# Performance work log

Measured on AMD Instinct MI355X. Metric: run time of the kernel, lower is better.

The kernel has to match this reference:

```python
import jax, jax.numpy as jnp
import numpy as np

N_NODES = 100000
N_EDGES = 1600000
NUM_FEATURES = 512
HIDDEN = 128
NUM_CLASSES = 40


def setup_inputs() -> dict:
    key = jax.random.key(0)
    ks = jax.random.split(key, 6)
    x = jax.random.normal(ks[0], (N_NODES, NUM_FEATURES), dtype=jnp.float32)
    edge_index = jax.random.randint(ks[1], (2, N_EDGES), 0, N_NODES, dtype=jnp.int32)
    W1 = jax.random.normal(ks[2], (NUM_FEATURES, HIDDEN), dtype=jnp.float32) * 0.05
    b1 = jnp.zeros((HIDDEN,), dtype=jnp.float32)
    W2 = jax.random.normal(ks[3], (HIDDEN, NUM_CLASSES), dtype=jnp.float32) * 0.05
    b2 = jnp.zeros((NUM_CLASSES,), dtype=jnp.float32)
    return {"x": x, "edge_index": edge_index, "W1": W1, "b1": b1, "W2": W2, "b2": b2}


def _gcn_conv(x, W, b, src, dst, n):
    # PyG GCNConv: h = W x; out = D^{-1/2} (A + I) D^{-1/2} h + b
    h = x @ W                                            # [N, out]
    deg = jax.ops.segment_sum(jnp.ones(src.shape[0], h.dtype), dst,
                              num_segments=n) + 1.0      # +1 for self loop
    inv_sqrt = jax.lax.rsqrt(deg)                        # [N]
    coef = inv_sqrt[src] * inv_sqrt[dst]                 # [E]
    msgs = h[src] * coef[:, None]                        # [E, out] gather
    agg = jax.ops.segment_sum(msgs, dst, num_segments=n) # scatter-add
    agg = agg + h * (inv_sqrt * inv_sqrt)[:, None]       # self-loop term
    return agg + b


def reference(x, edge_index, W1, b1, W2, b2):
    src, dst = edge_index[0], edge_index[1]
    n = x.shape[0]
    h = jax.nn.relu(_gcn_conv(x, W1, b1, src, dst, n))
    # F.dropout(training=self.training): eval mode -> identity
    out = _gcn_conv(h, W2, b2, src, dst, n)
    return jax.nn.log_softmax(out, axis=1)
```

## Files before the change

### kernel.cpp

```cpp
#include <hip/hip_runtime.h>
#include <hip/hip_bf16.h>
#include <math.h>

#define N_NODES 100000
#define N_EDGES 1600000
#define F_IN 512
#define HID 128
#define NCLS 40
#define DEG_CAP 64
#define GM 128
#define NGB 782

typedef __attribute__((ext_vector_type(8))) short short8;
typedef __attribute__((ext_vector_type(4))) float floatx4;

__device__ __forceinline__ unsigned short f2bf(float x) {
    unsigned u = __builtin_bit_cast(unsigned, x);
    unsigned r = (u + 0x7FFFu + ((u >> 16) & 1u)) >> 16;
    return (unsigned short)r;
}
__device__ __forceinline__ float bflo(unsigned u) {
    return __builtin_bit_cast(float, u << 16);
}
__device__ __forceinline__ float bfhi(unsigned u) {
    return __builtin_bit_cast(float, u & 0xFFFF0000u);
}


__global__ __launch_bounds__(256) void k_prep(
    const float* __restrict__ W1, unsigned short* __restrict__ W1t,
    const float* __restrict__ W2, unsigned short* __restrict__ W2th,
    unsigned short* __restrict__ W2tl, int* __restrict__ cursor) {
    int b = blockIdx.x;
    if (b < 256) {
        int idx = b * 256 + threadIdx.x;
        int n = idx >> 9, k = idx & 511;
        W1t[idx] = f2bf(W1[k * HID + n]);
    } else if (b < 280) {
        int idx = (b - 256) * 256 + threadIdx.x;
        int n = idx >> 7, k = idx & 127;
        float v = (n < NCLS) ? W2[k * NCLS + n] : 0.f;
        unsigned short hi = f2bf(v);
        unsigned short lo = f2bf(v - bflo(hi));
        W2th[idx] = hi;
        W2tl[idx] = lo;
    } else {
        int i = (b - 280) * 256 + threadIdx.x;
        if (i < N_NODES) cursor[i] = 0;
    }
}


__global__ __launch_bounds__(256) void k_fused_g1f(
    const float* __restrict__ A,
    const unsigned short* __restrict__ Bt,
    unsigned short* __restrict__ C,
    int M,
    const int* __restrict__ src, const int* __restrict__ dst,
    int* __restrict__ cursor, int* __restrict__ csr)
{
    __shared__ unsigned short Asl[128 * 40];
    __shared__ unsigned short Bsl[128 * 40];

    if (blockIdx.x >= NGB) {
        int i = (blockIdx.x - NGB) * 256 + threadIdx.x;
        int d = dst[i];
        int pos = atomicAdd(&cursor[d], 1);
        if (pos < DEG_CAP) csr[((size_t)d << 6) + pos] = src[i];
        return;
    }

    const int tid  = threadIdx.x;
    const int wave = tid >> 6;
    const int lane = tid & 63;
    const int quad = lane >> 4;
    const int l15  = lane & 15;
    const int wm   = (wave >> 1) * 64;
    const int wn   = (wave & 1) * 64;
    const int block_m = blockIdx.x * GM;

    floatx4 acc[4][4];
    #pragma unroll
    for (int i = 0; i < 4; ++i)
        #pragma unroll
        for (int j = 0; j < 4; ++j) acc[i][j] = (floatx4){0.f, 0.f, 0.f, 0.f};

    for (int k0 = 0; k0 < F_IN; k0 += 32) {
        #pragma unroll
        for (int i = 0; i < 4; ++i) {
            int f  = tid + 256 * i;
            int r  = f >> 3;
            int kq = f & 7;
            int gr = block_m + r;
            gr = gr < M ? gr : M - 1;
            floatx4 v = *(const floatx4*)&A[(size_t)gr * F_IN + k0 + kq * 4];
            unsigned lo = (unsigned)f2bf(v.x) | ((unsigned)f2bf(v.y) << 16);
            unsigned hi = (unsigned)f2bf(v.z) | ((unsigned)f2bf(v.w) << 16);
            *(uint2*)&Asl[r * 40 + kq * 4] = make_uint2(lo, hi);
        }
        #pragma unroll
        for (int i = 0; i < 2; ++i) {
            int f  = tid + 256 * i;
            int r  = f >> 2;
            int kq = f & 3;
            int4 v = *(const int4*)&Bt[(size_t)r * F_IN + k0 + kq * 8];
            *(int4*)&Bsl[r * 40 + kq * 8] = v;
        }
        __syncthreads();

        short8 af[4], bfr[4];
        #pragma unroll
        for (int t = 0; t < 4; ++t)
            af[t] = *(const short8*)&Asl[(wm + t * 16 + l15) * 40 + quad * 8];
        #pragma unroll
        for (int t = 0; t < 4; ++t)
            bfr[t] = *(const short8*)&Bsl[(wn + t * 16 + l15) * 40 + quad * 8];

        #pragma unroll
        for (int tm = 0; tm < 4; ++tm)
            #pragma unroll
            for (int tn = 0; tn < 4; ++tn)
                acc[tm][tn] = __builtin_amdgcn_mfma_f32_16x16x32_bf16(
                    af[tm], bfr[tn], acc[tm][tn], 0, 0, 0);
        __syncthreads();
    }

    #pragma unroll
    for (int tm = 0; tm < 4; ++tm) {
        #pragma unroll
        for (int r = 0; r < 4; ++r) {
            int row = block_m + wm + tm * 16 + quad * 4 + r;
            if (row < M) {
                #pragma unroll
                for (int tn = 0; tn < 4; ++tn)
                    C[(size_t)row * HID + wn + tn * 16 + l15] =
                        f2bf(acc[tm][tn][r]);
            }
        }
    }
}

__global__ void k_inv(const int* __restrict__ deg, float* __restrict__ inv, int n) {
    int i = blockIdx.x * blockDim.x + threadIdx.x;
    if (i < n) inv[i] = rsqrtf((float)deg[i] + 1.0f);
}


__global__ __launch_bounds__(256) void k_gather1(
    const unsigned* __restrict__ h1s,
    const int* __restrict__ deg,
    const float* __restrict__ inv, const int* __restrict__ csr,
    const float* __restrict__ b1, float* __restrict__ hrelu)
{
    const int wave = threadIdx.x >> 6;
    const int lane = threadIdx.x & 63;
    const int node = blockIdx.x * 4 + wave;
    const int start = node << 6;
    const float invd = inv[node];
    int cnt = deg[node];
    cnt = cnt < DEG_CAP ? cnt : DEG_CAP;

    unsigned u = h1s[(size_t)node * 64 + lane];
    float acc0 = bflo(u) * invd, acc1 = bfhi(u) * invd;

    int t = 0;
    for (; t + 4 <= cnt; t += 4) {
        int s0 = csr[start + t + 0];
        int s1 = csr[start + t + 1];
        int s2 = csr[start + t + 2];
        int s3 = csr[start + t + 3];
        float w0 = inv[s0], w1 = inv[s1], w2 = inv[s2], w3 = inv[s3];
        unsigned u0 = h1s[(size_t)s0 * 64 + lane];
        unsigned u1 = h1s[(size_t)s1 * 64 + lane];
        unsigned u2 = h1s[(size_t)s2 * 64 + lane];
        unsigned u3 = h1s[(size_t)s3 * 64 + lane];
        acc0 += (bflo(u0) * w0 + bflo(u1) * w1) + (bflo(u2) * w2 + bflo(u3) * w3);
        acc1 += (bfhi(u0) * w0 + bfhi(u1) * w1) + (bfhi(u2) * w2 + bfhi(u3) * w3);
    }
    for (; t < cnt; ++t) {
        int s = csr[start + t];
        float w = inv[s];
        unsigned uu = h1s[(size_t)s * 64 + lane];
        acc0 += bflo(uu) * w;
        acc1 += bfhi(uu) * w;
    }

    float2 b = *(const float2*)&b1[lane * 2];
    float v0 = fmaxf(acc0 * invd + b.x, 0.f);
    float v1 = fmaxf(acc1 * invd + b.y, 0.f);
    *(float2*)&hrelu[(size_t)node * HID + lane * 2] = make_float2(v0, v1);
}


#define G2M 128

__global__ __launch_bounds__(256) void k_gemm2_mfma(
    const float* __restrict__ H,
    const unsigned short* __restrict__ Bh,
    const unsigned short* __restrict__ Bl,
    const float* __restrict__ inv,
    unsigned short* __restrict__ C,
    int M)
{
    __shared__ unsigned short Ahs[128 * 40];
    __shared__ unsigned short Als[128 * 40];
    __shared__ unsigned short Bhs[48 * 136];
    __shared__ unsigned short Bls[48 * 136];

    const int tid  = threadIdx.x;
    const int wave = tid >> 6;
    const int lane = tid & 63;
    const int quad = lane >> 4;
    const int l15  = lane & 15;
    const int wm   = wave * 32;
    const int block_m = blockIdx.x * G2M;

    for (int i = tid; i < 768; i += 256) {
        int n = i >> 4;
        int k = (i & 15) * 8;
        *(int4*)&Bhs[n * 136 + k] = *(const int4*)&Bh[n * 128 + k];
        *(int4*)&Bls[n * 136 + k] = *(const int4*)&Bl[n * 128 + k];
    }

    const int ra = tid >> 3, kqa = tid & 7;
    size_t aoff[4];
    #pragma unroll
    for (int i = 0; i < 4; ++i) {
        int gr = block_m + ra + 32 * i;
        gr = gr < M ? gr : M - 1;
        aoff[i] = (size_t)gr * HID + kqa * 4;
    }

    floatx4 hreg[4];
    #pragma unroll
    for (int i = 0; i < 4; ++i) hreg[i] = *(const floatx4*)&H[aoff[i]];

    floatx4 acc[2][3];
    #pragma unroll
    for (int i = 0; i < 2; ++i)
        #pragma unroll
        for (int j = 0; j < 3; ++j) acc[i][j] = (floatx4){0.f, 0.f, 0.f, 0.f};

    for (int step = 0; step < 4; ++step) {
        #pragma unroll
        for (int i = 0; i < 4; ++i) {
            floatx4 v = hreg[i];
            unsigned short hx = f2bf(v.x), hy = f2bf(v.y);
            unsigned short hz = f2bf(v.z), hw = f2bf(v.w);
            unsigned short lx = f2bf(v.x - bflo(hx));
            unsigned short ly = f2bf(v.y - bflo(hy));
            unsigned short lz = f2bf(v.z - bflo(hz));
            unsigned short lw = f2bf(v.w - bflo(hw));
            *(uint2*)&Ahs[(ra + 32 * i) * 40 + kqa * 4] =
                make_uint2((unsigned)hx | ((unsigned)hy << 16),
                           (unsigned)hz | ((unsigned)hw << 16));
            *(uint2*)&Als[(ra + 32 * i) * 40 + kqa * 4] =
                make_uint2((unsigned)lx | ((unsigned)ly << 16),
                           (unsigned)lz | ((unsigned)lw << 16));
        }
        __syncthreads();

        if (step < 3) {
            const int k1 = (step + 1) * 32;
            #pragma unroll
            for (int i = 0; i < 4; ++i) hreg[i] = *(const floatx4*)&H[aoff[i] + k1];
        }

        const int k0 = step * 32;
        short8 ah[2], al[2], bh[3], bl[3];
        #pragma unroll
        for (int t = 0; t < 2; ++t) {
            ah[t] = *(const short8*)&Ahs[(wm + t * 16 + l15) * 40 + quad * 8];
            al[t] = *(const short8*)&Als[(wm + t * 16 + l15) * 40 + quad * 8];
        }
        #pragma unroll
        for (int t = 0; t < 3; ++t) {
            bh[t] = *(const short8*)&Bhs[(t * 16 + l15) * 136 + k0 + quad * 8];
            bl[t] = *(const short8*)&Bls[(t * 16 + l15) * 136 + k0 + quad * 8];
        }

        #pragma unroll
        for (int tm = 0; tm < 2; ++tm)
            #pragma unroll
            for (int tn = 0; tn < 3; ++tn) {
                acc[tm][tn] = __builtin_amdgcn_mfma_f32_16x16x32_bf16(
                    ah[tm], bh[tn], acc[tm][tn], 0, 0, 0);
                acc[tm][tn] = __builtin_amdgcn_mfma_f32_16x16x32_bf16(
                    al[tm], bh[tn], acc[tm][tn], 0, 0, 0);
                acc[tm][tn] = __builtin_amdgcn_mfma_f32_16x16x32_bf16(
                    ah[tm], bl[tn], acc[tm][tn], 0, 0, 0);
            }
        __syncthreads();
    }

    #pragma unroll
    for (int tm = 0; tm < 2; ++tm) {
        #pragma unroll
        for (int r = 0; r < 4; ++r) {
            int row = block_m + wm + tm * 16 + quad * 4 + r;
            if (row < M) {
                float iv = inv[row];
                #pragma unroll
                for (int tn = 0; tn < 3; ++tn) {
                    int col = tn * 16 + l15;
                    if (col < NCLS)
                        C[(size_t)row * NCLS + col] = f2bf(acc[tm][tn][r] * iv);
                }
            }
        }
    }
}


__global__ __launch_bounds__(256) void k_gather2(
    const unsigned* __restrict__ h2s,
    const int* __restrict__ deg,
    const float* __restrict__ inv, const int* __restrict__ csr,
    const float* __restrict__ b2, float* __restrict__ out)
{
    const int wave = threadIdx.x >> 6;
    const int lane = threadIdx.x & 63;
    const int node = blockIdx.x * 4 + wave;
    const int g = lane / 20;
    const int j = lane - g * 20;
    const int start = node << 6;
    int cnt = deg[node];
    cnt = cnt < DEG_CAP ? cnt : DEG_CAP;

    float acc0 = 0.f, acc1 = 0.f;
    if (g == 0) {
        unsigned u = h2s[(size_t)node * 20 + j];
        acc0 = bflo(u);
        acc1 = bfhi(u);
    }
    if (g < 3) {
        int t = g;
        for (; t + 3 < cnt; t += 6) {
            int s0 = csr[start + t];
            int s1 = csr[start + t + 3];
            unsigned u0 = h2s[(size_t)s0 * 20 + j];
            unsigned u1 = h2s[(size_t)s1 * 20 + j];
            acc0 += bflo(u0) + bflo(u1);
            acc1 += bfhi(u0) + bfhi(u1);
        }
        if (t < cnt) {
            int s = csr[start + t];
            unsigned u = h2s[(size_t)s * 20 + j];
            acc0 += bflo(u);
            acc1 += bfhi(u);
        }
    }
    acc0 += __shfl(acc0, j + 20) + __shfl(acc0, j + 40);
    acc1 += __shfl(acc1, j + 20) + __shfl(acc1, j + 40);

    float invd = inv[node];
    float v0 = -INFINITY, v1 = -INFINITY;
    if (g == 0) {
        float2 b = *(const float2*)&b2[j * 2];
        v0 = acc0 * invd + b.x;
        v1 = acc1 * invd + b.y;
    }
    float m = fmaxf(v0, v1);
    #pragma unroll
    for (int mask = 16; mask; mask >>= 1) m = fmaxf(m, __shfl_xor(m, mask));
    float e = (g == 0) ? (__expf(v0 - m) + __expf(v1 - m)) : 0.f;
    #pragma unroll
    for (int mask = 16; mask; mask >>= 1) e += __shfl_xor(e, mask);
    if (g == 0) {
        float lg = __logf(e);
        *(float2*)&out[(size_t)node * NCLS + j * 2] =
            make_float2(v0 - m - lg, v1 - m - lg);
    }
}


extern "C" void kernel_launch(void* const* d_in, const int* in_sizes, int n_in,
                              void* d_out, int out_size, void* d_ws, size_t ws_size,
                              hipStream_t stream) {
    const float* x   = (const float*)d_in[0];
    const int*   ei  = (const int*)d_in[1];
    const float* W1  = (const float*)d_in[2];
    const float* b1  = (const float*)d_in[3];
    const float* W2  = (const float*)d_in[4];
    const float* b2  = (const float*)d_in[5];
    float* out = (float*)d_out;

    const int* src = ei;
    const int* dst = ei + N_EDGES;

    char* wsb = (char*)d_ws;
    float* inv      = (float*)wsb;
    float* slot1    = inv + 131072;
    float* hrelu    = slot1 + (size_t)N_NODES * HID;
    int*   cursor   = (int*)(hrelu + (size_t)N_NODES * HID);
    int*   csr_pad  = cursor + 131072;
    unsigned short* W1t  = (unsigned short*)(csr_pad + (size_t)N_NODES * DEG_CAP);
    unsigned short* W2th = W1t + (size_t)F_IN * HID;
    unsigned short* W2tl = W2th + 48 * 128;
    unsigned short* h1s_st = (unsigned short*)slot1;
    unsigned short* h2s_st = (unsigned short*)slot1;
    unsigned* h1s_ld = (unsigned*)slot1;
    unsigned* h2s_ld = (unsigned*)slot1;

    const int T = 256;
    const int NB = (N_NODES + 255) / 256;

    k_prep<<<280 + NB, T, 0, stream>>>(W1, W1t, W2, W2th, W2tl, cursor);

    k_fused_g1f<<<NGB + N_EDGES / T, T, 0, stream>>>(
        x, W1t, h1s_st, N_NODES, src, dst, cursor, csr_pad);

    k_inv<<<NB, T, 0, stream>>>(cursor, inv, N_NODES);

    k_gather1<<<N_NODES / 4, T, 0, stream>>>(h1s_ld, cursor, inv, csr_pad, b1, hrelu);

    k_gemm2_mfma<<<(N_NODES + G2M - 1) / G2M, T, 0, stream>>>(hrelu, W2th, W2tl, inv, h2s_st, N_NODES);
    k_gather2<<<N_NODES / 4, T, 0, stream>>>(h2s_ld, cursor, inv, csr_pad, b2, out);
}
```

Baseline: 523.7 us.

## Drop inv kernel, compute rsqrt degree inline, reorder fused blocks, widen gather unroll

Removes the separate k_inv launch and the inv array, recomputing rsqrt(deg+1) inline from the cursor counts in gather1, gemm2 and gather2. The fused kernel now puts the edge-bucketing blocks first so they are scheduled before the GEMM blocks. gather1 loads CSR indices as int4 and unrolls its neighbour loop by 8 for more loads in flight. The cost is an extra rsqrt per neighbour and a gather from the int deg array in place of the float inv array.

```diff
diff --git a/kernel.cpp b/kernel.cpp
--- a/kernel.cpp
+++ b/kernel.cpp
@@ -9,7 +9,7 @@
 #define NCLS 40
 #define DEG_CAP 64
 #define GM 128
-#define NGB 782
+#define NFB 6250
 
 typedef __attribute__((ext_vector_type(8))) short short8;
 typedef __attribute__((ext_vector_type(4))) float floatx4;
@@ -24,6 +24,9 @@
 }
 __device__ __forceinline__ float bfhi(unsigned u) {
     return __builtin_bit_cast(float, u & 0xFFFF0000u);
+}
+__device__ __forceinline__ float dinv(int dg) {
+    return rsqrtf((float)dg + 1.0f);
 }
 
 
@@ -62,8 +65,8 @@
     __shared__ unsigned short Asl[128 * 40];
     __shared__ unsigned short Bsl[128 * 40];
 
-    if (blockIdx.x >= NGB) {
-        int i = (blockIdx.x - NGB) * 256 + threadIdx.x;
+    if (blockIdx.x < NFB) {
+        int i = blockIdx.x * 256 + threadIdx.x;
         int d = dst[i];
         int pos = atomicAdd(&cursor[d], 1);
         if (pos < DEG_CAP) csr[((size_t)d << 6) + pos] = src[i];
@@ -77,7 +80,7 @@
     const int l15  = lane & 15;
     const int wm   = (wave >> 1) * 64;
     const int wn   = (wave & 1) * 64;
-    const int block_m = blockIdx.x * GM;
+    const int block_m = (blockIdx.x - NFB) * GM;
 
     floatx4 acc[4][4];
     #pragma unroll
@@ -140,46 +143,59 @@
     }
 }
 
-__global__ void k_inv(const int* __restrict__ deg, float* __restrict__ inv, int n) {
-    int i = blockIdx.x * blockDim.x + threadIdx.x;
-    if (i < n) inv[i] = rsqrtf((float)deg[i] + 1.0f);
-}
-
 
 __global__ __launch_bounds__(256) void k_gather1(
     const unsigned* __restrict__ h1s,
     const int* __restrict__ deg,
-    const float* __restrict__ inv, const int* __restrict__ csr,
+    const int* __restrict__ csr,
     const float* __restrict__ b1, float* __restrict__ hrelu)
 {
     const int wave = threadIdx.x >> 6;
     const int lane = threadIdx.x & 63;
     const int node = blockIdx.x * 4 + wave;
     const int start = node << 6;
-    const float invd = inv[node];
-    int cnt = deg[node];
-    cnt = cnt < DEG_CAP ? cnt : DEG_CAP;
+    const int dgn = deg[node];
+    const float invd = dinv(dgn);
+    int cnt = dgn < DEG_CAP ? dgn : DEG_CAP;
 
     unsigned u = h1s[(size_t)node * 64 + lane];
     float acc0 = bflo(u) * invd, acc1 = bfhi(u) * invd;
 
     int t = 0;
-    for (; t + 4 <= cnt; t += 4) {
-        int s0 = csr[start + t + 0];
-        int s1 = csr[start + t + 1];
-        int s2 = csr[start + t + 2];
-        int s3 = csr[start + t + 3];
-        float w0 = inv[s0], w1 = inv[s1], w2 = inv[s2], w3 = inv[s3];
-        unsigned u0 = h1s[(size_t)s0 * 64 + lane];
-        unsigned u1 = h1s[(size_t)s1 * 64 + lane];
-        unsigned u2 = h1s[(size_t)s2 * 64 + lane];
-        unsigned u3 = h1s[(size_t)s3 * 64 + lane];
+    for (; t + 8 <= cnt; t += 8) {
+        int4 ia = *(const int4*)&csr[start + t];
+        int4 ib = *(const int4*)&csr[start + t + 4];
+        float w0 = dinv(deg[ia.x]), w1 = dinv(deg[ia.y]);
+        float w2 = dinv(deg[ia.z]), w3 = dinv(deg[ia.w]);
+        float w4 = dinv(deg[ib.x]), w5 = dinv(deg[ib.y]);
+        float w6 = dinv(deg[ib.z]), w7 = dinv(deg[ib.w]);
+        unsigned u0 = h1s[(size_t)ia.x * 64 + lane];
+        unsigned u1 = h1s[(size_t)ia.y * 64 + lane];
+        unsigned u2 = h1s[(size_t)ia.z * 64 + lane];
+        unsigned u3 = h1s[(size_t)ia.w * 64 + lane];
+        unsigned u4 = h1s[(size_t)ib.x * 64 + lane];
+        unsigned u5 = h1s[(size_t)ib.y * 64 + lane];
+        unsigned u6 = h1s[(size_t)ib.z * 64 + lane];
+        unsigned u7 = h1s[(size_t)ib.w * 64 + lane];
         acc0 += (bflo(u0) * w0 + bflo(u1) * w1) + (bflo(u2) * w2 + bflo(u3) * w3);
         acc1 += (bfhi(u0) * w0 + bfhi(u1) * w1) + (bfhi(u2) * w2 + bfhi(u3) * w3);
+        acc0 += (bflo(u4) * w4 + bflo(u5) * w5) + (bflo(u6) * w6 + bflo(u7) * w7);
+        acc1 += (bfhi(u4) * w4 + bfhi(u5) * w5) + (bfhi(u6) * w6 + bfhi(u7) * w7);
+    }
+    for (; t + 4 <= cnt; t += 4) {
+        int4 ia = *(const int4*)&csr[start + t];
+        float w0 = dinv(deg[ia.x]), w1 = dinv(deg[ia.y]);
+        float w2 = dinv(deg[ia.z]), w3 = dinv(deg[ia.w]);
+        unsigned u0 = h1s[(size_t)ia.x * 64 + lane];
+        unsigned u1 = h1s[(size_t)ia.y * 64 + lane];
+        unsigned u2 = h1s[(size_t)ia.z * 64 + lane];
+        unsigned u3 = h1s[(size_t)ia.w * 64 + lane];
+        acc0 += (bflo(u0) * w0 + bflo(u1) * w1) + (bflo(u2) * w2 + bflo(u3) * w3);
+        acc1 += (bfhi(u0) * w0 + bfhi(u1) * w1) + (bfhi(u2) * w2 + bfhi(u3) * w3);
     }
     for (; t < cnt; ++t) {
         int s = csr[start + t];
-        float w = inv[s];
+        float w = dinv(deg[s]);
         unsigned uu = h1s[(size_t)s * 64 + lane];
         acc0 += bflo(uu) * w;
         acc1 += bfhi(uu) * w;
@@ -198,7 +214,7 @@
     const float* __restrict__ H,
     const unsigned short* __restrict__ Bh,
     const unsigned short* __restrict__ Bl,
-    const float* __restrict__ inv,
+    const int* __restrict__ deg,
     unsigned short* __restrict__ C,
     int M)
 {
@@ -299,7 +315,7 @@
         for (int r = 0; r < 4; ++r) {
             int row = block_m + wm + tm * 16 + quad * 4 + r;
             if (row < M) {
-                float iv = inv[row];
+                float iv = dinv(deg[row]);
                 #pragma unroll
                 for (int tn = 0; tn < 3; ++tn) {
                     int col = tn * 16 + l15;
@@ -315,7 +331,7 @@
 __global__ __launch_bounds__(256) void k_gather2(
     const unsigned* __restrict__ h2s,
     const int* __restrict__ deg,
-    const float* __restrict__ inv, const int* __restrict__ csr,
+    const int* __restrict__ csr,
     const float* __restrict__ b2, float* __restrict__ out)
 {
     const int wave = threadIdx.x >> 6;
@@ -324,8 +340,8 @@
     const int g = lane / 20;
     const int j = lane - g * 20;
     const int start = node << 6;
-    int cnt = deg[node];
-    cnt = cnt < DEG_CAP ? cnt : DEG_CAP;
+    const int dgn = deg[node];
+    int cnt = dgn < DEG_CAP ? dgn : DEG_CAP;
 
     float acc0 = 0.f, acc1 = 0.f;
     if (g == 0) {
@@ -353,7 +369,7 @@
     acc0 += __shfl(acc0, j + 20) + __shfl(acc0, j + 40);
     acc1 += __shfl(acc1, j + 20) + __shfl(acc1, j + 40);
 
-    float invd = inv[node];
+    float invd = dinv(dgn);
     float v0 = -INFINITY, v1 = -INFINITY;
     if (g == 0) {
         float2 b = *(const float2*)&b2[j * 2];
@@ -389,8 +405,7 @@
     const int* dst = ei + N_EDGES;
 
     char* wsb = (char*)d_ws;
-    float* inv      = (float*)wsb;
-    float* slot1    = inv + 131072;
+    float* slot1    = (float*)wsb;
     float* hrelu    = slot1 + (size_t)N_NODES * HID;
     int*   cursor   = (int*)(hrelu + (size_t)N_NODES * HID);
     int*   csr_pad  = cursor + 131072;
@@ -407,13 +422,11 @@
 
     k_prep<<<280 + NB, T, 0, stream>>>(W1, W1t, W2, W2th, W2tl, cursor);
 
-    k_fused_g1f<<<NGB + N_EDGES / T, T, 0, stream>>>(
+    k_fused_g1f<<<NFB + (N_NODES + GM - 1) / GM, T, 0, stream>>>(
         x, W1t, h1s_st, N_NODES, src, dst, cursor, csr_pad);
 
-    k_inv<<<NB, T, 0, stream>>>(cursor, inv, N_NODES);
-
-    k_gather1<<<N_NODES / 4, T, 0, stream>>>(h1s_ld, cursor, inv, csr_pad, b1, hrelu);
-
-    k_gemm2_mfma<<<(N_NODES + G2M - 1) / G2M, T, 0, stream>>>(hrelu, W2th, W2tl, inv, h2s_st, N_NODES);
-    k_gather2<<<N_NODES / 4, T, 0, stream>>>(h2s_ld, cursor, inv, csr_pad, b2, out);
-}
+    k_gather1<<<N_NODES / 4, T, 0, stream>>>(h1s_ld, cursor, csr_pad, b1, hrelu);
+
+    k_gemm2_mfma<<<(N_NODES + G2M - 1) / G2M, T, 0, stream>>>(hrelu, W2th, W2tl, cursor, h2s_st, N_NODES);
+    k_gather2<<<N_NODES / 4, T, 0, stream>>>(h2s_ld, cursor, csr_pad, b2, out);
+}
```

Result: slower. 544.0 us (+3.9%).
